# Kernel tuning notes

Measured on AMD Instinct MI355X. Metric: run time of the kernel, lower is better.

The kernel has to match this reference:

```python
import jax, jax.numpy as jnp
import numpy as np

CHANNELS = 32
HIDDEN = 1024
LAYERS = 8
NODE_TYPES = 7
N_NODES = 500_000
N_EDGES = 2_000_000
NUM_GRAPHS = 1024


def setup_inputs() -> dict:
    key = jax.random.key(0)
    ks = jax.random.split(key, 8)
    nodes = jax.random.randint(ks[0], (N_NODES,), 0, NODE_TYPES)
    sources = jax.random.randint(ks[1], (N_EDGES,), 0, N_NODES)
    targets = jax.random.randint(ks[2], (N_EDGES,), 0, N_NODES)
    # sorted graph ids covering all NUM_GRAPHS graphs (no empty graphs)
    batch = (jnp.arange(N_NODES) * NUM_GRAPHS) // N_NODES
    emb = jax.random.normal(ks[3], (NODE_TYPES, CHANNELS), dtype=jnp.float32)
    # xavier-normal-ish init for the 8 layers x {out, back} 32x32 convs
    xavier_std = (2.0 / (CHANNELS + CHANNELS)) ** 0.5
    conv_w = jax.random.normal(ks[4], (LAYERS, 2, CHANNELS, CHANNELS), dtype=jnp.float32) * xavier_std
    hidden_w = jax.random.normal(ks[5], (CHANNELS, HIDDEN), dtype=jnp.float32) * 0.05
    hidden_b = jax.random.normal(ks[6], (HIDDEN,), dtype=jnp.float32) * 0.05
    out_w = jax.random.normal(ks[7], (HIDDEN, 1), dtype=jnp.float32) * 0.05
    return dict(nodes=nodes, sources=sources, targets=targets, batch=batch,
                emb=emb, conv_w=conv_w, hidden_w=hidden_w, hidden_b=hidden_b,
                out_w=out_w)


def reference(nodes, sources, targets, batch, emb, conv_w, hidden_w, hidden_b, out_w):
    n = nodes.shape[0]
    ones_e = jnp.ones(sources.shape[0], dtype=jnp.float32)
    # norm = 1 / (1 + in-degree), norm_t = 1 / (1 + out-degree)  [N,1]
    norm = (1.0 / (1.0 + jax.ops.segment_sum(ones_e, targets, num_segments=n)))[:, None]
    norm_t = (1.0 / (1.0 + jax.ops.segment_sum(ones_e, sources, num_segments=n)))[:, None]
    node_counts = jax.ops.segment_sum(jnp.ones(n, dtype=jnp.float32), batch,
                                      num_segments=NUM_GRAPHS)

    x = emb[nodes]  # [N, C]

    def conv(x, s, t, nrm, w):
        # x.index_add(0, t, x[s]) -> x + scatter_add of gathered source feats
        agg = nrm * (x + jax.ops.segment_sum(x[s], t, num_segments=n))
        return jax.nn.relu(agg @ w)

    for l in range(LAYERS):
        x = x + conv(x, sources, targets, norm, conv_w[l, 0]) \
              + conv(x, targets, sources, norm_t, conv_w[l, 1])

    # mean pooling per graph
    g = jax.ops.segment_sum(x, batch, num_segments=NUM_GRAPHS) / node_counts[:, None]
    h = jax.nn.relu(g @ hidden_w + hidden_b)
    return (h @ out_w).squeeze(-1)  # [NUM_GRAPHS]
```

## Files before the change

kernel.cpp:

```cpp
#include <hip/hip_runtime.h>

#define CHANNELS 32
#define HIDDEN 1024
#define LAYERS 8
#define NRANGE 8

typedef __attribute__((ext_vector_type(8))) short short8;
typedef __attribute__((ext_vector_type(4))) float float4v;

__device__ __forceinline__ short f2bf_rne(float f) {
    union { float f; unsigned u; } v; v.f = f;
    unsigned r = v.u + 0x7fffu + ((v.u >> 16) & 1u);
    return (short)(r >> 16);
}
__device__ __forceinline__ float bf2f(short h) {
    union { float f; unsigned u; } v; v.u = ((unsigned)(unsigned short)h) << 16;
    return v.f;
}
__device__ __forceinline__ float bfu2f(unsigned short h) {
    union { float f; unsigned u; } v; v.u = ((unsigned)h) << 16;
    return v.f;
}
__device__ __forceinline__ float bflo(unsigned u) {
    union { float f; unsigned u; } v; v.u = u << 16; return v.f;
}
__device__ __forceinline__ float bfhi(unsigned u) {
    union { float f; unsigned u; } v; v.u = u & 0xffff0000u; return v.f;
}
__device__ __forceinline__ unsigned packbf(float x, float y) {
    return ((unsigned)(unsigned short)f2bf_rne(y) << 16) |
            (unsigned)(unsigned short)f2bf_rne(x);
}


__global__ __launch_bounds__(256)
void pre_kernel(const int* __restrict__ src, const int* __restrict__ tgt,
                int* __restrict__ deg2,
                const int* __restrict__ nodes, const float* __restrict__ emb,
                unsigned short* __restrict__ hi0, unsigned short* __restrict__ lo,
                const int* __restrict__ batch, float* __restrict__ counts,
                int n_nodes, int n_edges, int n_graphs, int rsh,
                int degB, int initB) {
    int bid = blockIdx.x;
    int tid = threadIdx.x;
    if (bid < degB) {
        int r = bid & (NRANGE - 1);
        int chunk = bid >> 3;
        int base = chunk * 2048;
#pragma unroll
        for (int j = 0; j < 8; j++) {
            int e = base + j * 256 + tid;
            if (e < n_edges) {
                int t = __builtin_nontemporal_load(tgt + e);
                int s = __builtin_nontemporal_load(src + e);
                if ((t >> rsh) == r) atomicAdd(&deg2[t], 1);
                if ((s >> rsh) == r) atomicAdd(&deg2[n_nodes + s], 1);
            }
        }
    } else if (bid < degB + initB) {
        int gid = (bid - degB) * 256 + tid;
        int i = gid >> 2, c8 = (gid & 3) * 8;
        if (i < n_nodes) {
            const float* e = emb + nodes[i] * CHANNELS + c8;
            short8 hv, lv;
#pragma unroll
            for (int k = 0; k < 8; k++) {
                float v = e[k];
                short hsh = f2bf_rne(v);
                hv[k] = hsh;
                lv[k] = f2bf_rne(v - bf2f(hsh));
            }
            *(short8*)(hi0 + (size_t)i * CHANNELS + c8) = hv;
            *(short8*)(lo  + (size_t)i * CHANNELS + c8) = lv;
        }
    } else {
        int b = (bid - degB - initB) * 256 + tid;
        if (b < n_graphs) {
            int lo_i = 0, hi_i = n_nodes;
            while (lo_i < hi_i) { int mid = (lo_i + hi_i) >> 1; if (batch[mid] < b) lo_i = mid + 1; else hi_i = mid; }
            int s0 = lo_i;
            lo_i = 0; hi_i = n_nodes;
            while (lo_i < hi_i) { int mid = (lo_i + hi_i) >> 1; if (batch[mid] < b + 1) lo_i = mid + 1; else hi_i = mid; }
            counts[b] = (float)(lo_i - s0);
        }
    }
}


__global__ __launch_bounds__(256)
void scan_pass1(const int* __restrict__ deg, int* __restrict__ bs, int n) {
    __shared__ int sh[256];
    int t = threadIdx.x;
    int base = blockIdx.x * 2048 + t * 8;
    int s = 0;
#pragma unroll
    for (int j = 0; j < 8; j++) { int idx = base + j; if (idx < n) s += deg[idx]; }
    sh[t] = s; __syncthreads();
    for (int st = 128; st > 0; st >>= 1) { if (t < st) sh[t] += sh[t + st]; __syncthreads(); }
    if (t == 0) bs[blockIdx.x] = sh[0];
}

__global__ void scan_pass2(int* __restrict__ bs, int nb) {
    __shared__ int sh[1024];
    int t = threadIdx.x;
    int v = (t < nb) ? bs[t] : 0;
    sh[t] = v; __syncthreads();
    for (int off = 1; off < 1024; off <<= 1) {
        int u = (t >= off) ? sh[t - off] : 0; __syncthreads();
        sh[t] += u; __syncthreads();
    }
    if (t < nb) bs[t] = sh[t] - v;
}

__global__ __launch_bounds__(256)
void scan_pass3(const int* __restrict__ deg, const int* __restrict__ bs,
                int* __restrict__ off, int* __restrict__ cur, int n) {
    __shared__ int sh[256];
    int t = threadIdx.x;
    int base = blockIdx.x * 2048 + t * 8;
    int v[8]; int s = 0;
#pragma unroll
    for (int j = 0; j < 8; j++) { int idx = base + j; v[j] = (idx < n) ? deg[idx] : 0; s += v[j]; }
    sh[t] = s; __syncthreads();
    for (int st = 1; st < 256; st <<= 1) {
        int u = (t >= st) ? sh[t - st] : 0; __syncthreads();
        sh[t] += u; __syncthreads();
    }
    int acc = bs[blockIdx.x] + sh[t] - s;
#pragma unroll
    for (int j = 0; j < 8; j++) {
        int idx = base + j;
        if (idx < n) { off[idx] = acc; cur[idx] = acc; }
        acc += v[j];
    }
}


__global__ __launch_bounds__(256)
void scatter_range_kernel(const int* __restrict__ src, const int* __restrict__ tgt,
                          int* __restrict__ cur2, int* __restrict__ nbr,
                          int n_nodes, int n_edges, int rsh, int rbase) {
    int r = rbase + (blockIdx.x & (NRANGE - 1));
    int chunk = blockIdx.x >> 3;
    int base = chunk * 2048;
#pragma unroll
    for (int j = 0; j < 8; j++) {
        int e = base + j * 256 + threadIdx.x;
        if (e < n_edges) {
            int t = __builtin_nontemporal_load(tgt + e);
            int s = __builtin_nontemporal_load(src + e);
            if ((t >> rsh) == r) { int p = atomicAdd(&cur2[t], 1);           nbr[p] = s; }
            if ((s >> rsh) == r) { int q = atomicAdd(&cur2[n_nodes + s], 1); nbr[q] = t; }
        }
    }
}


__global__ __launch_bounds__(256, 8)
void layer_mfma(const int* __restrict__ off2, const int* __restrict__ nbr,
                const float* __restrict__ wbase,
                const unsigned short* __restrict__ hi_in,
                unsigned short* __restrict__ hi_out,
                unsigned short* __restrict__ lo,
                int n_nodes, int n_edges) {
    __shared__ short A1h[64][32], A2h[64][32];
    __shared__ short W0h[32][32], W1h[32][32];
    __shared__ int offIn[65], offOut[65];

    int tid = threadIdx.x;
    int nodeblock = blockIdx.x * 64;

    for (int idx = tid; idx < CHANNELS * CHANNELS; idx += 256) {
        int k = idx >> 5, n = idx & 31;
        W0h[n][k] = f2bf_rne(wbase[idx]);
        W1h[n][k] = f2bf_rne(wbase[CHANNELS * CHANNELS + idx]);
    }
    if (tid < 65) {
        int idx = nodeblock + tid;
        offIn[tid]  = (idx <= n_nodes) ? off2[idx] : n_edges;
        int idx2 = n_nodes + idx;
        offOut[tid] = (idx2 < 2 * n_nodes) ? off2[idx2] : 2 * n_edges;
    }
    __syncthreads();

    int c = tid & 31, g = tid >> 5;
    int h = c >> 4;
    int cc = c & 15;

    int bi_c, d1_c, bo_c, d2_c, nbl1_c, nbl2_c, node_c;
    float xvx_c, xvy_c;
    {
        int local = g;
        node_c = nodeblock + local;
        bi_c = offIn[local];  d1_c = offIn[local + 1] - bi_c;
        bo_c = offOut[local]; d2_c = offOut[local + 1] - bo_c;
        nbl1_c = (c < d1_c) ? nbr[bi_c + c] : 0;
        nbl2_c = (c < d2_c) ? nbr[bo_c + c] : 0;
        xvx_c = 0.f; xvy_c = 0.f;
        if (node_c < n_nodes) {
            unsigned hp = *(const unsigned*)(hi_in + (size_t)node_c * CHANNELS + 2 * cc);
            unsigned lp = *(const unsigned*)(lo    + (size_t)node_c * CHANNELS + 2 * cc);
            xvx_c = bflo(hp) + bflo(lp);
            xvy_c = bfhi(hp) + bfhi(lp);
        }
    }

    for (int pass = 0; pass < 8; pass++) {
        int bi_n = 0, d1_n = 0, bo_n = 0, d2_n = 0, nbl1_n = 0, nbl2_n = 0, node_n = 0;
        float xvx_n = 0.f, xvy_n = 0.f;
        if (pass < 7) {
            int local = (pass + 1) * 8 + g;
            node_n = nodeblock + local;
            bi_n = offIn[local];  d1_n = offIn[local + 1] - bi_n;
            bo_n = offOut[local]; d2_n = offOut[local + 1] - bo_n;
            nbl1_n = (c < d1_n) ? nbr[bi_n + c] : 0;
            nbl2_n = (c < d2_n) ? nbr[bo_n + c] : 0;
            if (node_n < n_nodes) {
                unsigned hp = *(const unsigned*)(hi_in + (size_t)node_n * CHANNELS + 2 * cc);
                unsigned lp = *(const unsigned*)(lo    + (size_t)node_n * CHANNELS + 2 * cc);
                xvx_n = bflo(hp) + bflo(lp);
                xvy_n = bfhi(hp) + bfhi(lp);
            }
        }

        int local = pass * 8 + g;
        int i = node_c;
        int self = (i < n_nodes) ? i : 0;

        int m1 = d1_c < 32 ? d1_c : 32;
        int m2 = d2_c < 32 ? d2_c : 32;
        int mm = m1 > m2 ? m1 : m2;

        float s1x = 0.f, s1y = 0.f, s2x = 0.f, s2y = 0.f;
        for (int j = 0; j < mm; j += 4) {
            int sl0 = j + h;
            int sl1 = j + 2 + h;
            int p0 = __shfl(nbl1_c, sl0 & 31, 32);
            int p1 = __shfl(nbl1_c, sl1 & 31, 32);
            int q0 = __shfl(nbl2_c, sl0 & 31, 32);
            int q1 = __shfl(nbl2_c, sl1 & 31, 32);
            bool v10 = sl0 < m1, v11 = sl1 < m1;
            bool v20 = sl0 < m2, v21 = sl1 < m2;
            p0 = v10 ? p0 : self;
            p1 = v11 ? p1 : self;
            q0 = v20 ? q0 : self;
            q1 = v21 ? q1 : self;
            unsigned u0 = *(const unsigned*)(hi_in + (size_t)p0 * CHANNELS + 2 * cc);
            unsigned u1 = *(const unsigned*)(hi_in + (size_t)p1 * CHANNELS + 2 * cc);
            unsigned w0 = *(const unsigned*)(hi_in + (size_t)q0 * CHANNELS + 2 * cc);
            unsigned w1 = *(const unsigned*)(hi_in + (size_t)q1 * CHANNELS + 2 * cc);
            s1x += v10 ? bflo(u0) : 0.f;
            s1y += v10 ? bfhi(u0) : 0.f;
            s1x += v11 ? bflo(u1) : 0.f;
            s1y += v11 ? bfhi(u1) : 0.f;
            s2x += v20 ? bflo(w0) : 0.f;
            s2y += v20 ? bfhi(w0) : 0.f;
            s2x += v21 ? bflo(w1) : 0.f;
            s2y += v21 ? bfhi(w1) : 0.f;
        }
        s1x += __shfl_xor(s1x, 16, 32);
        s1y += __shfl_xor(s1y, 16, 32);
        s2x += __shfl_xor(s2x, 16, 32);
        s2y += __shfl_xor(s2y, 16, 32);

        for (int e = bi_c + 32; e < bi_c + d1_c; e++) {
            unsigned u = *(const unsigned*)(hi_in + (size_t)nbr[e] * CHANNELS + 2 * cc);
            s1x += bflo(u); s1y += bfhi(u);
        }
        for (int e = bo_c + 32; e < bo_c + d2_c; e++) {
            unsigned u = *(const unsigned*)(hi_in + (size_t)nbr[e] * CHANNELS + 2 * cc);
            s2x += bflo(u); s2y += bfhi(u);
        }

        unsigned pk1 = 0, pk2 = 0;
        if (i < n_nodes) {
            float n1 = 1.0f / (1.0f + (float)d1_c);
            float n2 = 1.0f / (1.0f + (float)d2_c);
            pk1 = packbf(n1 * (xvx_c + s1x), n1 * (xvy_c + s1y));
            pk2 = packbf(n2 * (xvx_c + s2x), n2 * (xvy_c + s2y));
        }
        unsigned* dst = (h == 0) ? (unsigned*)&A1h[local][2 * cc]
                                 : (unsigned*)&A2h[local][2 * cc];
        *dst = (h == 0) ? pk1 : pk2;

        bi_c = bi_n; d1_c = d1_n; bo_c = bo_n; d2_c = d2_n;
        nbl1_c = nbl1_n; nbl2_c = nbl2_n;
        xvx_c = xvx_n; xvy_c = xvy_n; node_c = node_n;
    }
    __syncthreads();

    int wv = tid >> 6, lane = tid & 63;
    int m = lane & 15, quad = lane >> 4;
    int row0 = wv * 16;

    short8 a1h = *(const short8*)&A1h[row0 + m][quad * 8];
    short8 a2h = *(const short8*)&A2h[row0 + m][quad * 8];

    float4v dd[4];
#pragma unroll
    for (int hh = 0; hh < 2; hh++) {
        int n0 = hh * 16 + m;
        short8 b0h = *(const short8*)&W0h[n0][quad * 8];
        short8 b1h = *(const short8*)&W1h[n0][quad * 8];
        float4v d1 = {0.f, 0.f, 0.f, 0.f};
        d1 = __builtin_amdgcn_mfma_f32_16x16x32_bf16(a1h, b0h, d1, 0, 0, 0);
        float4v d2 = {0.f, 0.f, 0.f, 0.f};
        d2 = __builtin_amdgcn_mfma_f32_16x16x32_bf16(a2h, b1h, d2, 0, 0, 0);
        dd[hh * 2] = d1; dd[hh * 2 + 1] = d2;
    }

#pragma unroll
    for (int hh = 0; hh < 2; hh++) {
        float4v d1 = dd[hh * 2], d2 = dd[hh * 2 + 1];
#pragma unroll
        for (int r = 0; r < 4; r++) {
            int local = row0 + quad * 4 + r;
            int node = nodeblock + local;
            if (node < n_nodes) {
                int col = hh * 16 + m;
                size_t idx = (size_t)node * CHANNELS + col;
                float base = bfu2f(hi_in[idx]) + bfu2f(lo[idx]);
                float v = base + fmaxf(d1[r], 0.f) + fmaxf(d2[r], 0.f);
                short hn = f2bf_rne(v);
                hi_out[idx] = (unsigned short)hn;
                lo[idx]     = (unsigned short)f2bf_rne(v - bf2f(hn));
            }
        }
    }
}


#define POOL_CHUNK 2048

__global__ __launch_bounds__(256)
void pool_kernel(const int* __restrict__ batch,
                 const unsigned short* __restrict__ hi,
                 const unsigned short* __restrict__ lo,
                 float* __restrict__ g, int n_nodes) {
    int c = threadIdx.x & 31;
    int r = threadIdx.x >> 5;
    int base = blockIdx.x * POOL_CHUNK;
    float acc = 0.f;
    int cur = -1;
    for (int it = 0; it < POOL_CHUNK / 8; it++) {
        int node = base + it * 8 + r;
        if (node >= n_nodes) break;
        int b = batch[node];
        if (b != cur) {
            if (cur >= 0) atomicAdd(&g[cur * CHANNELS + c], acc);
            acc = 0.f;
            cur = b;
        }
        size_t idx = (size_t)node * CHANNELS + c;
        acc += bfu2f(hi[idx]) + bfu2f(lo[idx]);
    }
    if (cur >= 0) atomicAdd(&g[cur * CHANNELS + c], acc);
}


__global__ __launch_bounds__(256)
void mlp_kernel(const float* __restrict__ g, const float* __restrict__ counts,
                const float* __restrict__ hidden_w, const float* __restrict__ hidden_b,
                const float* __restrict__ out_w, float* __restrict__ out) {
    __shared__ float grow[CHANNELS];
    __shared__ float red[256];
    int graph = blockIdx.x;
    int tid = threadIdx.x;
    if (tid < CHANNELS) grow[tid] = g[graph * CHANNELS + tid] / counts[graph];
    __syncthreads();
    float partial = 0.f;
    for (int q = 0; q < HIDDEN / 256; q++) {
        int j = q * 256 + tid;
        float h = hidden_b[j];
#pragma unroll
        for (int k = 0; k < CHANNELS; k++) h += grow[k] * hidden_w[k * HIDDEN + j];
        partial += fmaxf(h, 0.f) * out_w[j];
    }
    red[tid] = partial;
    __syncthreads();
    for (int s = 128; s > 0; s >>= 1) {
        if (tid < s) red[tid] += red[tid + s];
        __syncthreads();
    }
    if (tid == 0) out[graph] = red[0];
}


extern "C" void kernel_launch(void* const* d_in, const int* in_sizes, int n_in,
                              void* d_out, int out_size, void* d_ws, size_t ws_size,
                              hipStream_t stream) {
    const int*   nodes    = (const int*)d_in[0];
    const int*   sources  = (const int*)d_in[1];
    const int*   targets  = (const int*)d_in[2];
    const int*   batch    = (const int*)d_in[3];
    const float* emb      = (const float*)d_in[4];
    const float* conv_w   = (const float*)d_in[5];
    const float* hidden_w = (const float*)d_in[6];
    const float* hidden_b = (const float*)d_in[7];
    const float* out_w    = (const float*)d_in[8];
    float* out = (float*)d_out;

    const int n_nodes  = in_sizes[0];
    const int n_edges  = in_sizes[1];
    const int n_graphs = out_size;
    const int n2 = 2 * n_nodes;

    int rsh8 = 0;
    while (((n_nodes - 1) >> rsh8) >= 8) rsh8++;
    int rsh16 = 0;
    while (((n_nodes - 1) >> rsh16) >= 16) rsh16++;

    char* ws = (char*)d_ws;
    unsigned short* hi0 = (unsigned short*)ws; ws += (size_t)n_nodes * CHANNELS * 2;
    unsigned short* hi1 = (unsigned short*)ws; ws += (size_t)n_nodes * CHANNELS * 2;
    unsigned short* lo  = (unsigned short*)ws; ws += (size_t)n_nodes * CHANNELS * 2;
    int*   deg2   = (int*)ws;   ws += (size_t)n2 * 4;
    int*   off2   = (int*)ws;   ws += (size_t)n2 * 4;
    int*   cur2   = (int*)ws;   ws += (size_t)n2 * 4;
    int*   nbr    = (int*)ws;   ws += (size_t)2 * n_edges * 4;
    int*   bsums  = (int*)ws;   ws += 4096;
    float* g      = (float*)ws; ws += (size_t)n_graphs * CHANNELS * 4;
    float* counts = (float*)ws; ws += (size_t)n_graphs * 4;

    hipMemsetAsync(deg2, 0, (size_t)n2 * 4, stream);
    hipMemsetAsync(g, 0, (size_t)n_graphs * CHANNELS * 4, stream);

    int echunks = (n_edges + 2047) / 2048;
    int degB  = echunks * NRANGE;
    int initB = (n_nodes * 4 + 255) / 256;
    int cntB  = (n_graphs + 255) / 256;

    pre_kernel<<<degB + initB + cntB, 256, 0, stream>>>(sources, targets, deg2,
                                                        nodes, emb, hi0, lo,
                                                        batch, counts,
                                                        n_nodes, n_edges, n_graphs,
                                                        rsh8, degB, initB);

    int nblk = (n2 + 2047) / 2048;
    scan_pass1<<<nblk, 256, 0, stream>>>(deg2, bsums, n2);
    scan_pass2<<<1, 1024, 0, stream>>>(bsums, nblk);
    scan_pass3<<<nblk, 256, 0, stream>>>(deg2, bsums, off2, cur2, n2);

    scatter_range_kernel<<<echunks * NRANGE, 256, 0, stream>>>(sources, targets, cur2, nbr,
                                                               n_nodes, n_edges, rsh16, 0);
    scatter_range_kernel<<<echunks * NRANGE, 256, 0, stream>>>(sources, targets, cur2, nbr,
                                                               n_nodes, n_edges, rsh16, 8);

    unsigned short* hin = hi0; unsigned short* hout = hi1;
    int lblocks = (n_nodes + 63) / 64;
    for (int l = 0; l < LAYERS; l++) {
        const float* wbase = conv_w + (size_t)l * 2 * CHANNELS * CHANNELS;
        layer_mfma<<<lblocks, 256, 0, stream>>>(off2, nbr, wbase,
                                                hin, hout, lo, n_nodes, n_edges);
        unsigned short* tmp = hin; hin = hout; hout = tmp;
    }

    int pool_blocks = (n_nodes + POOL_CHUNK - 1) / POOL_CHUNK;
    pool_kernel<<<pool_blocks, 256, 0, stream>>>(batch, hin, lo, g, n_nodes);
    mlp_kernel<<<n_graphs, 256, 0, stream>>>(g, counts, hidden_w, hidden_b, out_w, out);
}
```

Baseline: 1.486 ms.

## Record per-edge atomic ranks during degree count to build CSR without second atomic pass

The degree-counting pass now keeps the return value of each atomicAdd as the edge's rank within its node's bucket and writes it to two per-edge arrays. A new placement kernel computes each neighbor slot as offset plus rank, with no atomics. This replaces the two range-partitioned atomic scatter passes and drops the cursor array. The range partitioning in the degree pass is also removed, so every edge is read once instead of once per range, at the cost of 16 MB more workspace traffic and atomics that are no longer localized by range.

Result: faster. 1.424 ms (-4.2%).

```diff
diff --git a/kernel.cpp b/kernel.cpp
--- a/kernel.cpp
+++ b/kernel.cpp
@@ -3,7 +3,6 @@
 #define CHANNELS 32
 #define HIDDEN 1024
 #define LAYERS 8
-#define NRANGE 8
 
 typedef __attribute__((ext_vector_type(8))) short short8;
 typedef __attribute__((ext_vector_type(4))) float float4v;
@@ -36,25 +35,26 @@
 __global__ __launch_bounds__(256)
 void pre_kernel(const int* __restrict__ src, const int* __restrict__ tgt,
                 int* __restrict__ deg2,
+                int* __restrict__ rank1, int* __restrict__ rank2,
                 const int* __restrict__ nodes, const float* __restrict__ emb,
                 unsigned short* __restrict__ hi0, unsigned short* __restrict__ lo,
                 const int* __restrict__ batch, float* __restrict__ counts,
-                int n_nodes, int n_edges, int n_graphs, int rsh,
+                int n_nodes, int n_edges, int n_graphs,
                 int degB, int initB) {
     int bid = blockIdx.x;
     int tid = threadIdx.x;
     if (bid < degB) {
-        int r = bid & (NRANGE - 1);
-        int chunk = bid >> 3;
-        int base = chunk * 2048;
+        int base = bid * 2048;
 #pragma unroll
         for (int j = 0; j < 8; j++) {
             int e = base + j * 256 + tid;
             if (e < n_edges) {
                 int t = __builtin_nontemporal_load(tgt + e);
                 int s = __builtin_nontemporal_load(src + e);
-                if ((t >> rsh) == r) atomicAdd(&deg2[t], 1);
-                if ((s >> rsh) == r) atomicAdd(&deg2[n_nodes + s], 1);
+                int r1 = atomicAdd(&deg2[t], 1);
+                int r2 = atomicAdd(&deg2[n_nodes + s], 1);
+                __builtin_nontemporal_store(r1, rank1 + e);
+                __builtin_nontemporal_store(r2, rank2 + e);
             }
         }
     } else if (bid < degB + initB) {
@@ -114,7 +114,7 @@
 
 __global__ __launch_bounds__(256)
 void scan_pass3(const int* __restrict__ deg, const int* __restrict__ bs,
-                int* __restrict__ off, int* __restrict__ cur, int n) {
+                int* __restrict__ off, int n) {
     __shared__ int sh[256];
     int t = threadIdx.x;
     int base = blockIdx.x * 2048 + t * 8;
@@ -130,27 +130,28 @@
 #pragma unroll
     for (int j = 0; j < 8; j++) {
         int idx = base + j;
-        if (idx < n) { off[idx] = acc; cur[idx] = acc; }
+        if (idx < n) off[idx] = acc;
         acc += v[j];
     }
 }
 
 
 __global__ __launch_bounds__(256)
-void scatter_range_kernel(const int* __restrict__ src, const int* __restrict__ tgt,
-                          int* __restrict__ cur2, int* __restrict__ nbr,
-                          int n_nodes, int n_edges, int rsh, int rbase) {
-    int r = rbase + (blockIdx.x & (NRANGE - 1));
-    int chunk = blockIdx.x >> 3;
-    int base = chunk * 2048;
+void place_kernel(const int* __restrict__ src, const int* __restrict__ tgt,
+                  const int* __restrict__ off2,
+                  const int* __restrict__ rank1, const int* __restrict__ rank2,
+                  int* __restrict__ nbr, int n_nodes, int n_edges) {
+    int base = blockIdx.x * 2048;
 #pragma unroll
     for (int j = 0; j < 8; j++) {
         int e = base + j * 256 + threadIdx.x;
         if (e < n_edges) {
             int t = __builtin_nontemporal_load(tgt + e);
             int s = __builtin_nontemporal_load(src + e);
-            if ((t >> rsh) == r) { int p = atomicAdd(&cur2[t], 1);           nbr[p] = s; }
-            if ((s >> rsh) == r) { int q = atomicAdd(&cur2[n_nodes + s], 1); nbr[q] = t; }
+            int r1 = __builtin_nontemporal_load(rank1 + e);
+            int r2 = __builtin_nontemporal_load(rank2 + e);
+            nbr[off2[t] + r1] = s;
+            nbr[off2[n_nodes + s] + r2] = t;
         }
     }
 }
@@ -405,18 +406,14 @@
     const int n_graphs = out_size;
     const int n2 = 2 * n_nodes;
 
-    int rsh8 = 0;
-    while (((n_nodes - 1) >> rsh8) >= 8) rsh8++;
-    int rsh16 = 0;
-    while (((n_nodes - 1) >> rsh16) >= 16) rsh16++;
-
     char* ws = (char*)d_ws;
     unsigned short* hi0 = (unsigned short*)ws; ws += (size_t)n_nodes * CHANNELS * 2;
     unsigned short* hi1 = (unsigned short*)ws; ws += (size_t)n_nodes * CHANNELS * 2;
     unsigned short* lo  = (unsigned short*)ws; ws += (size_t)n_nodes * CHANNELS * 2;
     int*   deg2   = (int*)ws;   ws += (size_t)n2 * 4;
     int*   off2   = (int*)ws;   ws += (size_t)n2 * 4;
-    int*   cur2   = (int*)ws;   ws += (size_t)n2 * 4;
+    int*   rank1  = (int*)ws;   ws += (size_t)n_edges * 4;
+    int*   rank2  = (int*)ws;   ws += (size_t)n_edges * 4;
     int*   nbr    = (int*)ws;   ws += (size_t)2 * n_edges * 4;
     int*   bsums  = (int*)ws;   ws += 4096;
     float* g      = (float*)ws; ws += (size_t)n_graphs * CHANNELS * 4;
@@ -426,25 +423,24 @@
     hipMemsetAsync(g, 0, (size_t)n_graphs * CHANNELS * 4, stream);
 
     int echunks = (n_edges + 2047) / 2048;
-    int degB  = echunks * NRANGE;
+    int degB  = echunks;
     int initB = (n_nodes * 4 + 255) / 256;
     int cntB  = (n_graphs + 255) / 256;
 
     pre_kernel<<<degB + initB + cntB, 256, 0, stream>>>(sources, targets, deg2,
+                                                        rank1, rank2,
                                                         nodes, emb, hi0, lo,
                                                         batch, counts,
                                                         n_nodes, n_edges, n_graphs,
-                                                        rsh8, degB, initB);
+                                                        degB, initB);
 
     int nblk = (n2 + 2047) / 2048;
     scan_pass1<<<nblk, 256, 0, stream>>>(deg2, bsums, n2);
     scan_pass2<<<1, 1024, 0, stream>>>(bsums, nblk);
-    scan_pass3<<<nblk, 256, 0, stream>>>(deg2, bsums, off2, cur2, n2);
-
-    scatter_range_kernel<<<echunks * NRANGE, 256, 0, stream>>>(sources, targets, cur2, nbr,
-                                                               n_nodes, n_edges, rsh16, 0);
-    scatter_range_kernel<<<echunks * NRANGE, 256, 0, stream>>>(sources, targets, cur2, nbr,
-                                                               n_nodes, n_edges, rsh16, 8);
+    scan_pass3<<<nblk, 256, 0, stream>>>(deg2, bsums, off2, n2);
+
+    place_kernel<<<echunks, 256, 0, stream>>>(sources, targets, off2,
+                                              rank1, rank2, nbr, n_nodes, n_edges);
 
     unsigned short* hin = hi0; unsigned short* hout = hi1;
     int lblocks = (n_nodes + 63) / 64;
```
